# Performance work log

Hardware: AMD Instinct MI355X
Metric: run time of the kernel (lower is better)

Reference implementation:

```python
import jax, jax.numpy as jnp
import numpy as np

N = 50000      # nodes
E = 400000     # edges (before self-loops)
IN = 128       # in_channels
OUT = 64       # out_channels (per-head; concat=False averages heads)
HEADS = 8      # heads of first GAT layer; second layer has 1 head
NEG_SLOPE = 0.2


def _glorot(key, shape, fan_in, fan_out):
    s = jnp.sqrt(2.0 / (fan_in + fan_out)).astype(jnp.float32)
    return jax.random.normal(key, shape, jnp.float32) * s


def setup_inputs() -> dict:
    key = jax.random.key(0)
    ks = jax.random.split(key, 10)
    x = jax.random.normal(ks[0], (N, IN), jnp.float32)
    edge_index = jax.random.randint(ks[1], (2, E), 0, N)
    # layer 1: heads=HEADS, per-head dim OUT
    W1 = _glorot(ks[2], (IN, HEADS * OUT), IN, HEADS * OUT)
    att_src1 = _glorot(ks[3], (HEADS, OUT), OUT, 1)
    att_dst1 = _glorot(ks[4], (HEADS, OUT), OUT, 1)
    b1 = jnp.zeros((OUT,), jnp.float32)
    # layer 2: heads=1
    W2 = _glorot(ks[5], (OUT, 1 * OUT), OUT, OUT)
    att_src2 = _glorot(ks[6], (1, OUT), OUT, 1)
    att_dst2 = _glorot(ks[7], (1, OUT), OUT, 1)
    b2 = jnp.zeros((OUT,), jnp.float32)
    return dict(x=x, edge_index=edge_index, W1=W1, att_src1=att_src1,
                att_dst1=att_dst1, b1=b1, W2=W2, att_src2=att_src2,
                att_dst2=att_dst2, b2=b2)


def gat_conv(x, edge_index, W, att_src, att_dst, bias, heads, ch):
    """PyG GATConv with concat=False (mean over heads), add_self_loops=True."""
    n = x.shape[0]
    loop = jnp.arange(n, dtype=edge_index.dtype)
    src = jnp.concatenate([edge_index[0], loop])  # [E+N]
    dst = jnp.concatenate([edge_index[1], loop])
    h = (x @ W).reshape(n, heads, ch)                     # [N, H, C]
    a_s = jnp.sum(h * att_src, axis=-1)                   # [N, H]
    a_d = jnp.sum(h * att_dst, axis=-1)                   # [N, H]
    e = jax.nn.leaky_relu(a_s[src] + a_d[dst], NEG_SLOPE)  # [E+N, H]
    # numerically stable segment softmax over incoming edges of each dst node
    emax = jax.lax.stop_gradient(
        jax.ops.segment_max(e, dst, num_segments=n))       # [N, H]
    ee = jnp.exp(e - emax[dst])
    denom = jax.ops.segment_sum(ee, dst, num_segments=n)  # [N, H]
    alpha = ee / denom[dst]                                # [E+N, H]
    out = jax.ops.segment_sum(alpha[:, :, None] * h[src], dst,
                              num_segments=n)              # [N, H, C]
    return out.mean(axis=1) + bias                         # [N, C]


def reference(x, edge_index, W1, att_src1, att_dst1, b1,
              W2, att_src2, att_dst2, b2):
    h = gat_conv(x, edge_index, W1, att_src1, att_dst1, b1, HEADS, OUT)
    h = jax.nn.elu(h)
    return gat_conv(h, edge_index, W2, att_src2, att_dst2, b2, 1, OUT)
```

## Files before the change

### kernel.cpp

```cpp
#include <hip/hip_runtime.h>
#include <cstdint>
#include <cstddef>

#define NEG_SLOPE 0.2f

typedef short bf16x8 __attribute__((ext_vector_type(8)));
typedef float f32x4 __attribute__((ext_vector_type(4)));
typedef float f32x2 __attribute__((ext_vector_type(2)));

__device__ __forceinline__ unsigned short f2bf(float f) {
  unsigned u = __float_as_uint(f);
  u = u + 0x7FFFu + ((u >> 16) & 1u);
  return (unsigned short)(u >> 16);
}
__device__ __forceinline__ float bf2f(unsigned short b) {
  return __uint_as_float((unsigned)b << 16);
}
__device__ __forceinline__ f32x2 unpk(unsigned xv) {
  f32x2 r;
  r.x = __uint_as_float(xv << 16);
  r.y = __uint_as_float(xv & 0xFFFF0000u);
  return r;
}
__device__ __forceinline__ float rlf(float v, int l) {
  return __uint_as_float(
      (unsigned)__builtin_amdgcn_readlane((int)__float_as_uint(v), l));
}

__global__ __launch_bounds__(256) void prep_all(
    const int* __restrict__ ei, int* __restrict__ counts,
    int* __restrict__ posb,
    const float* __restrict__ x, unsigned short* __restrict__ xb,
    const float* __restrict__ W1, const float* __restrict__ att_s1,
    const float* __restrict__ att_d1, unsigned short* __restrict__ AsAdT,
    unsigned short* __restrict__ WbT,
    const float* __restrict__ W2, unsigned short* __restrict__ W2t,
    const float* __restrict__ att_s2, const float* __restrict__ att_d2,
    float* __restrict__ AsAd2,
    int E, int ET, int N, int B0, int B1) {
  int b = blockIdx.x, tid = threadIdx.x;
  if (b < B0) {
    int i = b * 256 + tid;
    if (i < ET) {
      int dst = (i < E) ? ei[E + i] : (i - E);
      int pos = atomicAdd(&counts[dst], 1);
      posb[i] = pos;
    }
    return;
  }
  b -= B0;
  if (b < B1) {
    int i = b * 256 + tid;
    if (i < N * 32) {
      float4 v = ((const float4*)x)[i];
      ushort4 o;
      o.x = f2bf(v.x); o.y = f2bf(v.y); o.z = f2bf(v.z); o.w = f2bf(v.w);
      ((ushort4*)xb)[i] = o;
    }
    return;
  }
  b -= B1;
  if (b < 8) {
    int i = b * 256 + tid;
    int o = i >> 7, k = i & 127, h = o & 7;
    const float* att = (o < 8) ? att_s1 : att_d1;
    float s = 0.f;
    for (int c = 0; c < 64; c++) s += W1[(size_t)k * 512 + h * 64 + c] * att[h * 64 + c];
    AsAdT[i] = f2bf(s);
    return;
  }
  b -= 8;
  if (b < 256) {
    int i = b * 256 + tid;
    int o = i >> 10, k = i & 1023, h = k >> 7, c = k & 127;
    WbT[i] = f2bf(W1[(size_t)c * 512 + h * 64 + o]);
    return;
  }
  b -= 256;
  if (b < 16) {
    int i = b * 256 + tid;
    if (i < 64 * 64) {
      int k = i >> 6, nn = i & 63;
      W2t[(size_t)nn * 64 + k] = f2bf(W2[i]);
    }
    return;
  }
  {
    int i = tid;
    if (i < 128) {
      int o = i >> 6, k = i & 63;
      const float* att = (o == 0) ? att_s2 : att_d2;
      float s = 0.f;
      for (int c = 0; c < 64; c++) s += W2[(size_t)k * 64 + c] * att[c];
      AsAd2[i] = s;
    }
  }
}

__global__ __launch_bounds__(1024) void scan_dots(
    const int* __restrict__ counts, int* __restrict__ offsets,
    const unsigned short* __restrict__ xb, const unsigned short* __restrict__ AsAdT,
    float* __restrict__ asd, int n) {
  if (blockIdx.x == 0) {
    __shared__ int sums[1024];
    int t = threadIdx.x;
    int chunk = (n + 1023) >> 10;
    int start = t * chunk;
    int end = min(start + chunk, n);
    int s = 0;
    for (int i = start; i < end; i++) s += counts[i];
    sums[t] = s;
    __syncthreads();
    for (int off = 1; off < 1024; off <<= 1) {
      int v = (t >= off) ? sums[t - off] : 0;
      __syncthreads();
      sums[t] += v;
      __syncthreads();
    }
    int run = sums[t] - s;
    for (int i = start; i < end; i++) { offsets[i] = run; run += counts[i]; }
    if (t == 1023) offsets[n] = sums[1023];
    return;
  }
  int tid = threadIdx.x;
  int wave = tid >> 6, lane = tid & 63;
  int q = lane >> 4, t = lane & 15;
  int row0 = (blockIdx.x - 1) * 256 + wave * 16;
  int arow = row0 + t; if (arow > n - 1) arow = n - 1;
  const bf16x8* aptr = (const bf16x8*)(xb + (size_t)arow * 128);
  const bf16x8* bptr = (const bf16x8*)(AsAdT + t * 128);
  f32x4 acc = (f32x4){0.f, 0.f, 0.f, 0.f};
  #pragma unroll
  for (int s = 0; s < 4; s++)
    acc = __builtin_amdgcn_mfma_f32_16x16x32_bf16(aptr[s * 4 + q], bptr[s * 4 + q],
                                                  acc, 0, 0, 0);
  #pragma unroll
  for (int r = 0; r < 4; r++) {
    int row = row0 + q * 4 + r;
    if (row < n) asd[row * 16 + t] = acc[r];
  }
}

__global__ __launch_bounds__(256) void fill_csr(
    const int* __restrict__ ei, const int* __restrict__ offsets,
    const int* __restrict__ posb, int* __restrict__ srcs, int E, int ET) {
  int i = blockIdx.x * 256 + threadIdx.x;
  if (i >= ET) return;
  int src, dst;
  if (i < E) { src = ei[i]; dst = ei[E + i]; } else { src = dst = i - E; }
  srcs[offsets[dst] + posb[i]] = src;
}

#define CONSUME8R(RV, W, ACC)                                         \
  _Pragma("unroll")                                                   \
  for (int k = 0; k < 8; k++) {                                       \
    f32x2 x2 = unpk(RV[k]);                                           \
    ACC[0] += x2 * rlf(W, k * 8 + 0);                                 \
    ACC[1] += x2 * rlf(W, k * 8 + 1);                                 \
    ACC[2] += x2 * rlf(W, k * 8 + 2);                                 \
    ACC[3] += x2 * rlf(W, k * 8 + 3);                                 \
    ACC[4] += x2 * rlf(W, k * 8 + 4);                                 \
    ACC[5] += x2 * rlf(W, k * 8 + 5);                                 \
    ACC[6] += x2 * rlf(W, k * 8 + 6);                                 \
    ACC[7] += x2 * rlf(W, k * 8 + 7);                                 \
  }

__global__ __launch_bounds__(1024, 8) void agg1_gemm(
    const int* __restrict__ offsets, const int* __restrict__ srcs,
    const float* __restrict__ asd, const unsigned short* __restrict__ xb,
    const unsigned short* __restrict__ WbT, const float* __restrict__ b1,
    const float* __restrict__ AsAd2, unsigned short* __restrict__ zb,
    float* __restrict__ as2, float* __restrict__ ad2, int N) {
  __shared__ unsigned short sh[16 * 1032];
  int tid = threadIdx.x;
  int wv = tid >> 6, lane = tid & 63;
  int nb = blockIdx.x;
  {
    int node = nb * 16 + wv;
    f32x2 acc[8];
    #pragma unroll
    for (int h = 0; h < 8; h++) acc[h] = (f32x2){0.f, 0.f};
    float wsl = 0.f;
    int beg = offsets[node], end = offsets[node + 1];
    int jl = end - 1;
    float adv = asd[(size_t)node * 16 + 8 + (lane & 7)];
    for (int cb = beg; cb < end; cb += 16) {
      int cnt = min(16, end - cb);
      int sAll = srcs[min(cb + (lane & 15), jl)];
      int swa = srcs[min(cb + (lane >> 3), jl)];
      float asva = asd[(size_t)swa * 16 + (lane & 7)];
      float asvb = 0.f;
      if (cnt > 8) {
        int swb = srcs[min(cb + 8 + (lane >> 3), jl)];
        asvb = asd[(size_t)swb * 16 + (lane & 7)];
      }
      unsigned rva[8], rvb[8];
      #pragma unroll
      for (int k = 0; k < 8; k++) {
        int se = __builtin_amdgcn_readlane(sAll, k);
        rva[k] = *(const unsigned*)&xb[(size_t)(unsigned)se * 128 + 2 * lane];
      }
      if (cnt > 8) {
        #pragma unroll
        for (int k = 0; k < 8; k++) {
          int se = __builtin_amdgcn_readlane(sAll, k + 8);
          rvb[k] = *(const unsigned*)&xb[(size_t)(unsigned)se * 128 + 2 * lane];
        }
      }
      float wa, wb = 0.f;
      {
        float v = asva + adv;
        v = (v > 0.f) ? v : NEG_SLOPE * v;
        wa = (cb + (lane >> 3) < end) ? __expf(v) : 0.f;
      }
      if (cnt > 8) {
        float v = asvb + adv;
        v = (v > 0.f) ? v : NEG_SLOPE * v;
        wb = (cb + 8 + (lane >> 3) < end) ? __expf(v) : 0.f;
      }
      wsl += wa + wb;
      CONSUME8R(rva, wa, acc);
      if (cnt > 8) { CONSUME8R(rvb, wb, acc); }
    }
    wsl += __shfl_xor(wsl, 8, 64);
    wsl += __shfl_xor(wsl, 16, 64);
    wsl += __shfl_xor(wsl, 32, 64);
    #pragma unroll
    for (int h = 0; h < 8; h++) {
      float tot = rlf(wsl, h);
      float iv = 0.125f / tot;
      unsigned o = (unsigned)f2bf(acc[h].x * iv) | ((unsigned)f2bf(acc[h].y * iv) << 16);
      *(unsigned*)&sh[wv * 1032 + h * 128 + 2 * lane] = o;
    }
  }
  __syncthreads();
  if (wv < 4) {
    int q = lane >> 4, t = lane & 15;
    f32x4 acc4 = (f32x4){0.f, 0.f, 0.f, 0.f};
    const unsigned short* bbase = WbT + (size_t)(wv * 16 + t) * 1024;
    #pragma unroll 8
    for (int s = 0; s < 32; s++) {
      bf16x8 af = *(const bf16x8*)&sh[t * 1032 + s * 32 + q * 8];
      bf16x8 bf = *(const bf16x8*)&bbase[s * 32 + q * 8];
      acc4 = __builtin_amdgcn_mfma_f32_16x16x32_bf16(af, bf, acc4, 0, 0, 0);
    }
    int col = wv * 16 + t;
    float bias = b1[col];
    float vs = AsAd2[col], vd = AsAd2[64 + col];
    #pragma unroll
    for (int r = 0; r < 4; r++) {
      int row = q * 4 + r;
      int node = nb * 16 + row;
      float v = acc4[r] + bias;
      v = (v > 0.f) ? v : (__expf(v) - 1.f);
      zb[(size_t)node * 64 + col] = f2bf(v);
      float s = v * vs, d = v * vd;
      #pragma unroll
      for (int off = 1; off < 16; off <<= 1) {
        s += __shfl_xor(s, off, 64);
        d += __shfl_xor(d, off, 64);
      }
      if (t == 0) {
        atomicAdd(&as2[node], s);
        atomicAdd(&ad2[node], d);
      }
    }
  }
}

__global__ __launch_bounds__(1024, 8) void agg2_gemm(
    const int* __restrict__ offsets, const int* __restrict__ srcs,
    const float* __restrict__ as2, const float* __restrict__ ad2,
    const unsigned short* __restrict__ zb, const unsigned short* __restrict__ W2t,
    const float* __restrict__ b2, float* __restrict__ out, int N) {
  __shared__ unsigned short sh[16 * 72];
  int tid = threadIdx.x;
  int wv = tid >> 6, lane = tid & 63;
  int nb = blockIdx.x;
  {
    int node = nb * 16 + wv;
    int half = lane >> 5;
    float adv = ad2[node];
    int beg = offsets[node], end = offsets[node + 1];
    int jl = end - 1;
    f32x2 acc = (f32x2){0.f, 0.f};
    float wsl = 0.f;
    for (int cb = beg; cb < end; cb += 16) {
      int cnt = min(16, end - cb);
      int sAll = srcs[min(cb + (lane & 15), jl)];
      float asv = as2[sAll];
      unsigned rv[8];
      #pragma unroll
      for (int k = 0; k < 4; k++) {
        int s0 = __builtin_amdgcn_readlane(sAll, 2 * k);
        int s1 = __builtin_amdgcn_readlane(sAll, 2 * k + 1);
        int se = half ? s1 : s0;
        rv[k] = *(const unsigned*)&zb[(size_t)(unsigned)se * 64 + 2 * (lane & 31)];
      }
      if (cnt > 8) {
        #pragma unroll
        for (int k = 4; k < 8; k++) {
          int s0 = __builtin_amdgcn_readlane(sAll, 2 * k);
          int s1 = __builtin_amdgcn_readlane(sAll, 2 * k + 1);
          int se = half ? s1 : s0;
          rv[k] = *(const unsigned*)&zb[(size_t)(unsigned)se * 64 + 2 * (lane & 31)];
        }
      }
      float v = asv + adv;
      v = (v > 0.f) ? v : NEG_SLOPE * v;
      float wl = (cb + (lane & 15) < end) ? __expf(v) : 0.f;
      if (lane < 16) wsl += wl;
      #pragma unroll
      for (int k = 0; k < 4; k++) {
        float w0 = rlf(wl, 2 * k);
        float w1 = rlf(wl, 2 * k + 1);
        float w = half ? w1 : w0;
        acc += unpk(rv[k]) * w;
      }
      if (cnt > 8) {
        #pragma unroll
        for (int k = 4; k < 8; k++) {
          float w0 = rlf(wl, 2 * k);
          float w1 = rlf(wl, 2 * k + 1);
          float w = half ? w1 : w0;
          acc += unpk(rv[k]) * w;
        }
      }
    }
    wsl += __shfl_xor(wsl, 1, 64);
    wsl += __shfl_xor(wsl, 2, 64);
    wsl += __shfl_xor(wsl, 4, 64);
    wsl += __shfl_xor(wsl, 8, 64);
    float tot = rlf(wsl, 0);
    acc.x += __shfl_xor(acc.x, 32, 64);
    acc.y += __shfl_xor(acc.y, 32, 64);
    if (lane < 32) {
      float inv = 1.f / tot;
      unsigned o = (unsigned)f2bf(acc.x * inv) | ((unsigned)f2bf(acc.y * inv) << 16);
      *(unsigned*)&sh[wv * 72 + 2 * lane] = o;
    }
  }
  __syncthreads();
  if (wv < 4) {
    int q = lane >> 4, t = lane & 15;
    f32x4 acc4 = (f32x4){0.f, 0.f, 0.f, 0.f};
    const unsigned short* bbase = W2t + (size_t)(wv * 16 + t) * 64;
    #pragma unroll
    for (int s = 0; s < 2; s++) {
      bf16x8 af = *(const bf16x8*)&sh[t * 72 + s * 32 + q * 8];
      bf16x8 bf = *(const bf16x8*)&bbase[s * 32 + q * 8];
      acc4 = __builtin_amdgcn_mfma_f32_16x16x32_bf16(af, bf, acc4, 0, 0, 0);
    }
    int col = wv * 16 + t;
    float bias = b2[col];
    #pragma unroll
    for (int r = 0; r < 4; r++) {
      int node = nb * 16 + q * 4 + r;
      if (node < N) out[(size_t)node * 64 + col] = acc4[r] + bias;
    }
  }
}

extern "C" void kernel_launch(void* const* d_in, const int* in_sizes, int n_in,
                              void* d_out, int out_size, void* d_ws, size_t ws_size,
                              hipStream_t stream) {
  const int IN = 128;
  const int N = in_sizes[0] / IN;
  const int E = in_sizes[1] / 2;
  const int ET = E + N;

  const float* x        = (const float*)d_in[0];
  const int*   ei       = (const int*)d_in[1];
  const float* W1       = (const float*)d_in[2];
  const float* att_src1 = (const float*)d_in[3];
  const float* att_dst1 = (const float*)d_in[4];
  const float* b1       = (const float*)d_in[5];
  const float* W2       = (const float*)d_in[6];
  const float* att_src2 = (const float*)d_in[7];
  const float* att_dst2 = (const float*)d_in[8];
  const float* b2       = (const float*)d_in[9];
  float* out = (float*)d_out;

  char* base = (char*)d_ws;
  size_t off = 0;
  auto alloc = [&](size_t bytes) -> char* {
    char* p = base + off;
    off = (off + bytes + 255) & ~(size_t)255;
    return p;
  };
  unsigned short* xb    = (unsigned short*)alloc((size_t)N * 128 * 2);
  unsigned short* AsAdT = (unsigned short*)alloc((size_t)16 * 128 * 2);
  unsigned short* WbT   = (unsigned short*)alloc((size_t)64 * 1024 * 2);
  unsigned short* W2t   = (unsigned short*)alloc((size_t)64 * 64 * 2);
  unsigned short* zb    = (unsigned short*)alloc((size_t)N * 64 * 2);
  float* AsAd2 = (float*)alloc((size_t)128 * 4);
  float* asd1  = (float*)alloc((size_t)N * 16 * 4);
  int* offsets = (int*)alloc((size_t)(N + 1) * 4);
  int* srcs    = (int*)alloc((size_t)ET * 4);
  int* posb    = (int*)alloc((size_t)ET * 4);
  char* zero_begin = base + off;
  int* counts  = (int*)alloc((size_t)N * 4);
  float* a_s2  = (float*)alloc((size_t)N * 4);
  float* a_d2  = (float*)alloc((size_t)N * 4);
  char* zero_end = base + off;

  hipMemsetAsync(zero_begin, 0, (size_t)(zero_end - zero_begin), stream);

  const int TB = 256;
  auto cdiv = [](int a, int b) { return (a + b - 1) / b; };

  int B0 = cdiv(ET, TB);
  int B1 = cdiv(N * 32, TB);
  prep_all<<<B0 + B1 + 8 + 256 + 16 + 1, TB, 0, stream>>>(
      ei, counts, posb, x, xb, W1, att_src1, att_dst1, AsAdT, WbT, W2, W2t,
      att_src2, att_dst2, AsAd2, E, ET, N, B0, B1);

  scan_dots<<<1 + cdiv(N, 256), 1024, 0, stream>>>(counts, offsets, xb, AsAdT,
                                                   asd1, N);

  fill_csr<<<cdiv(ET, TB), TB, 0, stream>>>(ei, offsets, posb, srcs, E, ET);

  agg1_gemm<<<cdiv(N, 16), 1024, 0, stream>>>(offsets, srcs, asd1, xb, WbT, b1,
                                              AsAd2, zb, a_s2, a_d2, N);

  agg2_gemm<<<cdiv(N, 16), 1024, 0, stream>>>(offsets, srcs, a_s2, a_d2, zb,
                                              W2t, b2, out, N);
}
```

Before: 305.1 us.

## Halve aggregation block size to 8 nodes and skip unused neighbor row loads

The two fused aggregate+GEMM kernels now use 512-thread blocks covering 8 destination nodes instead of 16. The MFMA tile still has 16 rows, so half the rows duplicate the shared-memory data and their results are masked off. Neighbor feature gathers are now done in groups of 4 and skipped when the chunk holds fewer edges, which avoids redundant clamped loads for low-degree nodes. The intent is to cut barrier wait on the slowest wave in a block and to save memory traffic, at the cost of wasting half of each MFMA tile and launching twice as many blocks.

```diff
diff --git a/kernel.cpp b/kernel.cpp
--- a/kernel.cpp
+++ b/kernel.cpp
@@ -165,18 +165,18 @@
     ACC[7] += x2 * rlf(W, k * 8 + 7);                                 \
   }
 
-__global__ __launch_bounds__(1024, 8) void agg1_gemm(
+__global__ __launch_bounds__(512, 8) void agg1_gemm(
     const int* __restrict__ offsets, const int* __restrict__ srcs,
     const float* __restrict__ asd, const unsigned short* __restrict__ xb,
     const unsigned short* __restrict__ WbT, const float* __restrict__ b1,
     const float* __restrict__ AsAd2, unsigned short* __restrict__ zb,
     float* __restrict__ as2, float* __restrict__ ad2, int N) {
-  __shared__ unsigned short sh[16 * 1032];
+  __shared__ unsigned short sh[8 * 1032];
   int tid = threadIdx.x;
   int wv = tid >> 6, lane = tid & 63;
   int nb = blockIdx.x;
   {
-    int node = nb * 16 + wv;
+    int node = nb * 8 + wv;
     f32x2 acc[8];
     #pragma unroll
     for (int h = 0; h < 8; h++) acc[h] = (f32x2){0.f, 0.f};
@@ -188,21 +188,36 @@
       int cnt = min(16, end - cb);
       int sAll = srcs[min(cb + (lane & 15), jl)];
       int swa = srcs[min(cb + (lane >> 3), jl)];
-      float asva = asd[(size_t)swa * 16 + (lane & 7)];
+      float asva = asd[(size_t)(unsigned)swa * 16 + (lane & 7)];
       float asvb = 0.f;
       if (cnt > 8) {
         int swb = srcs[min(cb + 8 + (lane >> 3), jl)];
-        asvb = asd[(size_t)swb * 16 + (lane & 7)];
-      }
-      unsigned rva[8], rvb[8];
+        asvb = asd[(size_t)(unsigned)swb * 16 + (lane & 7)];
+      }
+      unsigned rva[8] = {0, 0, 0, 0, 0, 0, 0, 0};
+      unsigned rvb[8] = {0, 0, 0, 0, 0, 0, 0, 0};
       #pragma unroll
-      for (int k = 0; k < 8; k++) {
+      for (int k = 0; k < 4; k++) {
         int se = __builtin_amdgcn_readlane(sAll, k);
         rva[k] = *(const unsigned*)&xb[(size_t)(unsigned)se * 128 + 2 * lane];
       }
+      if (cnt > 4) {
+        #pragma unroll
+        for (int k = 4; k < 8; k++) {
+          int se = __builtin_amdgcn_readlane(sAll, k);
+          rva[k] = *(const unsigned*)&xb[(size_t)(unsigned)se * 128 + 2 * lane];
+        }
+      }
       if (cnt > 8) {
         #pragma unroll
-        for (int k = 0; k < 8; k++) {
+        for (int k = 0; k < 4; k++) {
+          int se = __builtin_amdgcn_readlane(sAll, k + 8);
+          rvb[k] = *(const unsigned*)&xb[(size_t)(unsigned)se * 128 + 2 * lane];
+        }
+      }
+      if (cnt > 12) {
+        #pragma unroll
+        for (int k = 4; k < 8; k++) {
           int se = __builtin_amdgcn_readlane(sAll, k + 8);
           rvb[k] = *(const unsigned*)&xb[(size_t)(unsigned)se * 128 + 2 * lane];
         }
@@ -240,7 +255,7 @@
     const unsigned short* bbase = WbT + (size_t)(wv * 16 + t) * 1024;
     #pragma unroll 8
     for (int s = 0; s < 32; s++) {
-      bf16x8 af = *(const bf16x8*)&sh[t * 1032 + s * 32 + q * 8];
+      bf16x8 af = *(const bf16x8*)&sh[(t & 7) * 1032 + s * 32 + q * 8];
       bf16x8 bf = *(const bf16x8*)&bbase[s * 32 + q * 8];
       acc4 = __builtin_amdgcn_mfma_f32_16x16x32_bf16(af, bf, acc4, 0, 0, 0);
     }
@@ -250,35 +265,37 @@
     #pragma unroll
     for (int r = 0; r < 4; r++) {
       int row = q * 4 + r;
-      int node = nb * 16 + row;
       float v = acc4[r] + bias;
       v = (v > 0.f) ? v : (__expf(v) - 1.f);
-      zb[(size_t)node * 64 + col] = f2bf(v);
       float s = v * vs, d = v * vd;
       #pragma unroll
       for (int off = 1; off < 16; off <<= 1) {
         s += __shfl_xor(s, off, 64);
         d += __shfl_xor(d, off, 64);
       }
-      if (t == 0) {
-        atomicAdd(&as2[node], s);
-        atomicAdd(&ad2[node], d);
-      }
-    }
-  }
-}
-
-__global__ __launch_bounds__(1024, 8) void agg2_gemm(
+      if (row < 8) {
+        int node = nb * 8 + row;
+        zb[(size_t)node * 64 + col] = f2bf(v);
+        if (t == 0) {
+          atomicAdd(&as2[node], s);
+          atomicAdd(&ad2[node], d);
+        }
+      }
+    }
+  }
+}
+
+__global__ __launch_bounds__(512, 8) void agg2_gemm(
     const int* __restrict__ offsets, const int* __restrict__ srcs,
     const float* __restrict__ as2, const float* __restrict__ ad2,
     const unsigned short* __restrict__ zb, const unsigned short* __restrict__ W2t,
     const float* __restrict__ b2, float* __restrict__ out, int N) {
-  __shared__ unsigned short sh[16 * 72];
+  __shared__ unsigned short sh[8 * 72];
   int tid = threadIdx.x;
   int wv = tid >> 6, lane = tid & 63;
   int nb = blockIdx.x;
   {
-    int node = nb * 16 + wv;
+    int node = nb * 8 + wv;
     int half = lane >> 5;
     float adv = ad2[node];
     int beg = offsets[node], end = offsets[node + 1];
@@ -289,17 +306,35 @@
       int cnt = min(16, end - cb);
       int sAll = srcs[min(cb + (lane & 15), jl)];
       float asv = as2[sAll];
-      unsigned rv[8];
+      unsigned rv[8] = {0, 0, 0, 0, 0, 0, 0, 0};
       #pragma unroll
-      for (int k = 0; k < 4; k++) {
+      for (int k = 0; k < 2; k++) {
         int s0 = __builtin_amdgcn_readlane(sAll, 2 * k);
         int s1 = __builtin_amdgcn_readlane(sAll, 2 * k + 1);
         int se = half ? s1 : s0;
         rv[k] = *(const unsigned*)&zb[(size_t)(unsigned)se * 64 + 2 * (lane & 31)];
       }
+      if (cnt > 4) {
+        #pragma unroll
+        for (int k = 2; k < 4; k++) {
+          int s0 = __builtin_amdgcn_readlane(sAll, 2 * k);
+          int s1 = __builtin_amdgcn_readlane(sAll, 2 * k + 1);
+          int se = half ? s1 : s0;
+          rv[k] = *(const unsigned*)&zb[(size_t)(unsigned)se * 64 + 2 * (lane & 31)];
+        }
+      }
       if (cnt > 8) {
         #pragma unroll
-        for (int k = 4; k < 8; k++) {
+        for (int k = 4; k < 6; k++) {
+          int s0 = __builtin_amdgcn_readlane(sAll, 2 * k);
+          int s1 = __builtin_amdgcn_readlane(sAll, 2 * k + 1);
+          int se = half ? s1 : s0;
+          rv[k] = *(const unsigned*)&zb[(size_t)(unsigned)se * 64 + 2 * (lane & 31)];
+        }
+      }
+      if (cnt > 12) {
+        #pragma unroll
+        for (int k = 6; k < 8; k++) {
           int s0 = __builtin_amdgcn_readlane(sAll, 2 * k);
           int s1 = __builtin_amdgcn_readlane(sAll, 2 * k + 1);
           int se = half ? s1 : s0;
@@ -347,7 +382,7 @@
     const unsigned short* bbase = W2t + (size_t)(wv * 16 + t) * 64;
     #pragma unroll
     for (int s = 0; s < 2; s++) {
-      bf16x8 af = *(const bf16x8*)&sh[t * 72 + s * 32 + q * 8];
+      bf16x8 af = *(const bf16x8*)&sh[(t & 7) * 72 + s * 32 + q * 8];
       bf16x8 bf = *(const bf16x8*)&bbase[s * 32 + q * 8];
       acc4 = __builtin_amdgcn_mfma_f32_16x16x32_bf16(af, bf, acc4, 0, 0, 0);
     }
@@ -355,8 +390,11 @@
     float bias = b2[col];
     #pragma unroll
     for (int r = 0; r < 4; r++) {
-      int node = nb * 16 + q * 4 + r;
-      if (node < N) out[(size_t)node * 64 + col] = acc4[r] + bias;
+      int row = q * 4 + r;
+      if (row < 8) {
+        int node = nb * 8 + row;
+        if (node < N) out[(size_t)node * 64 + col] = acc4[r] + bias;
+      }
     }
   }
 }
@@ -420,9 +458,9 @@
 
   fill_csr<<<cdiv(ET, TB), TB, 0, stream>>>(ei, offsets, posb, srcs, E, ET);
 
-  agg1_gemm<<<cdiv(N, 16), 1024, 0, stream>>>(offsets, srcs, asd1, xb, WbT, b1,
-                                              AsAd2, zb, a_s2, a_d2, N);
-
-  agg2_gemm<<<cdiv(N, 16), 1024, 0, stream>>>(offsets, srcs, a_s2, a_d2, zb,
-                                              W2t, b2, out, N);
-}
+  agg1_gemm<<<cdiv(N, 8), 512, 0, stream>>>(offsets, srcs, asd1, xb, WbT, b1,
+                                            AsAd2, zb, a_s2, a_d2, N);
+
+  agg2_gemm<<<cdiv(N, 8), 512, 0, stream>>>(offsets, srcs, a_s2, a_d2, zb,
+                                            W2t, b2, out, N);
+}
```

Result: slower. 338.8 us (+11.1%).

## Process four node groups per block in agg1_gemm with double-buffered shared tiles

Applied to the files above, without the earlier changes.

agg1_gemm now handles 64 nodes per block in four 16-node groups. Each group's gather-aggregation result goes into one of two shared buffers, and a different set of four waves runs the MFMA projection for each group. This lets the GEMM of one group overlap with the aggregation of the next and spreads the MFMA work across waves instead of leaving 12 waves idle. The cost is a larger shared-memory footprint, which may reduce occupancy, plus a __syncthreads per group, added node clamping and bounds guards.

```diff
diff --git a/kernel.cpp b/kernel.cpp
--- a/kernel.cpp
+++ b/kernel.cpp
@@ -171,98 +171,105 @@
     const unsigned short* __restrict__ WbT, const float* __restrict__ b1,
     const float* __restrict__ AsAd2, unsigned short* __restrict__ zb,
     float* __restrict__ as2, float* __restrict__ ad2, int N) {
-  __shared__ unsigned short sh[16 * 1032];
+  __shared__ unsigned short sh[2][16 * 1032];
   int tid = threadIdx.x;
   int wv = tid >> 6, lane = tid & 63;
-  int nb = blockIdx.x;
-  {
-    int node = nb * 16 + wv;
-    f32x2 acc[8];
-    #pragma unroll
-    for (int h = 0; h < 8; h++) acc[h] = (f32x2){0.f, 0.f};
-    float wsl = 0.f;
-    int beg = offsets[node], end = offsets[node + 1];
-    int jl = end - 1;
-    float adv = asd[(size_t)node * 16 + 8 + (lane & 7)];
-    for (int cb = beg; cb < end; cb += 16) {
-      int cnt = min(16, end - cb);
-      int sAll = srcs[min(cb + (lane & 15), jl)];
-      int swa = srcs[min(cb + (lane >> 3), jl)];
-      float asva = asd[(size_t)swa * 16 + (lane & 7)];
-      float asvb = 0.f;
-      if (cnt > 8) {
-        int swb = srcs[min(cb + 8 + (lane >> 3), jl)];
-        asvb = asd[(size_t)swb * 16 + (lane & 7)];
-      }
-      unsigned rva[8], rvb[8];
+  int nbase = blockIdx.x * 64;
+  for (int g = 0; g < 4; ++g) {
+    unsigned short* zt = &sh[g & 1][0];
+    {
+      int node = min(nbase + g * 16 + wv, N - 1);
+      f32x2 acc[8];
       #pragma unroll
-      for (int k = 0; k < 8; k++) {
-        int se = __builtin_amdgcn_readlane(sAll, k);
-        rva[k] = *(const unsigned*)&xb[(size_t)(unsigned)se * 128 + 2 * lane];
-      }
-      if (cnt > 8) {
+      for (int h = 0; h < 8; h++) acc[h] = (f32x2){0.f, 0.f};
+      float wsl = 0.f;
+      int beg = offsets[node], end = offsets[node + 1];
+      int jl = end - 1;
+      float adv = asd[(size_t)node * 16 + 8 + (lane & 7)];
+      for (int cb = beg; cb < end; cb += 16) {
+        int cnt = min(16, end - cb);
+        int sAll = srcs[min(cb + (lane & 15), jl)];
+        int swa = srcs[min(cb + (lane >> 3), jl)];
+        float asva = asd[(size_t)(unsigned)swa * 16 + (lane & 7)];
+        float asvb = 0.f;
+        if (cnt > 8) {
+          int swb = srcs[min(cb + 8 + (lane >> 3), jl)];
+          asvb = asd[(size_t)(unsigned)swb * 16 + (lane & 7)];
+        }
+        unsigned rva[8], rvb[8];
         #pragma unroll
         for (int k = 0; k < 8; k++) {
-          int se = __builtin_amdgcn_readlane(sAll, k + 8);
-          rvb[k] = *(const unsigned*)&xb[(size_t)(unsigned)se * 128 + 2 * lane];
-        }
-      }
-      float wa, wb = 0.f;
-      {
-        float v = asva + adv;
-        v = (v > 0.f) ? v : NEG_SLOPE * v;
-        wa = (cb + (lane >> 3) < end) ? __expf(v) : 0.f;
-      }
-      if (cnt > 8) {
-        float v = asvb + adv;
-        v = (v > 0.f) ? v : NEG_SLOPE * v;
-        wb = (cb + 8 + (lane >> 3) < end) ? __expf(v) : 0.f;
-      }
-      wsl += wa + wb;
-      CONSUME8R(rva, wa, acc);
-      if (cnt > 8) { CONSUME8R(rvb, wb, acc); }
-    }
-    wsl += __shfl_xor(wsl, 8, 64);
-    wsl += __shfl_xor(wsl, 16, 64);
-    wsl += __shfl_xor(wsl, 32, 64);
-    #pragma unroll
-    for (int h = 0; h < 8; h++) {
-      float tot = rlf(wsl, h);
-      float iv = 0.125f / tot;
-      unsigned o = (unsigned)f2bf(acc[h].x * iv) | ((unsigned)f2bf(acc[h].y * iv) << 16);
-      *(unsigned*)&sh[wv * 1032 + h * 128 + 2 * lane] = o;
-    }
-  }
-  __syncthreads();
-  if (wv < 4) {
-    int q = lane >> 4, t = lane & 15;
-    f32x4 acc4 = (f32x4){0.f, 0.f, 0.f, 0.f};
-    const unsigned short* bbase = WbT + (size_t)(wv * 16 + t) * 1024;
-    #pragma unroll 8
-    for (int s = 0; s < 32; s++) {
-      bf16x8 af = *(const bf16x8*)&sh[t * 1032 + s * 32 + q * 8];
-      bf16x8 bf = *(const bf16x8*)&bbase[s * 32 + q * 8];
-      acc4 = __builtin_amdgcn_mfma_f32_16x16x32_bf16(af, bf, acc4, 0, 0, 0);
-    }
-    int col = wv * 16 + t;
-    float bias = b1[col];
-    float vs = AsAd2[col], vd = AsAd2[64 + col];
-    #pragma unroll
-    for (int r = 0; r < 4; r++) {
-      int row = q * 4 + r;
-      int node = nb * 16 + row;
-      float v = acc4[r] + bias;
-      v = (v > 0.f) ? v : (__expf(v) - 1.f);
-      zb[(size_t)node * 64 + col] = f2bf(v);
-      float s = v * vs, d = v * vd;
+          int se = __builtin_amdgcn_readlane(sAll, k);
+          rva[k] = *(const unsigned*)&xb[(size_t)(unsigned)se * 128 + 2 * lane];
+        }
+        if (cnt > 8) {
+          #pragma unroll
+          for (int k = 0; k < 8; k++) {
+            int se = __builtin_amdgcn_readlane(sAll, k + 8);
+            rvb[k] = *(const unsigned*)&xb[(size_t)(unsigned)se * 128 + 2 * lane];
+          }
+        }
+        float wa, wb = 0.f;
+        {
+          float v = asva + adv;
+          v = (v > 0.f) ? v : NEG_SLOPE * v;
+          wa = (cb + (lane >> 3) < end) ? __expf(v) : 0.f;
+        }
+        if (cnt > 8) {
+          float v = asvb + adv;
+          v = (v > 0.f) ? v : NEG_SLOPE * v;
+          wb = (cb + 8 + (lane >> 3) < end) ? __expf(v) : 0.f;
+        }
+        wsl += wa + wb;
+        CONSUME8R(rva, wa, acc);
+        if (cnt > 8) { CONSUME8R(rvb, wb, acc); }
+      }
+      wsl += __shfl_xor(wsl, 8, 64);
+      wsl += __shfl_xor(wsl, 16, 64);
+      wsl += __shfl_xor(wsl, 32, 64);
       #pragma unroll
-      for (int off = 1; off < 16; off <<= 1) {
-        s += __shfl_xor(s, off, 64);
-        d += __shfl_xor(d, off, 64);
-      }
-      if (t == 0) {
-        atomicAdd(&as2[node], s);
-        atomicAdd(&ad2[node], d);
+      for (int h = 0; h < 8; h++) {
+        float tot = rlf(wsl, h);
+        float iv = 0.125f / tot;
+        unsigned o = (unsigned)f2bf(acc[h].x * iv) |
+                     ((unsigned)f2bf(acc[h].y * iv) << 16);
+        *(unsigned*)&zt[wv * 1032 + h * 128 + 2 * lane] = o;
+      }
+    }
+    __syncthreads();
+    if ((wv >> 2) == g) {
+      int w4 = wv & 3;
+      int q = lane >> 4, t = lane & 15;
+      f32x4 acc4 = (f32x4){0.f, 0.f, 0.f, 0.f};
+      const unsigned short* bbase = WbT + (size_t)(w4 * 16 + t) * 1024;
+      #pragma unroll 8
+      for (int s = 0; s < 32; s++) {
+        bf16x8 af = *(const bf16x8*)&zt[t * 1032 + s * 32 + q * 8];
+        bf16x8 bf = *(const bf16x8*)&bbase[s * 32 + q * 8];
+        acc4 = __builtin_amdgcn_mfma_f32_16x16x32_bf16(af, bf, acc4, 0, 0, 0);
+      }
+      int col = w4 * 16 + t;
+      float bias = b1[col];
+      float vs = AsAd2[col], vd = AsAd2[64 + col];
+      #pragma unroll
+      for (int r = 0; r < 4; r++) {
+        int row = q * 4 + r;
+        int node = nbase + g * 16 + row;
+        float v = acc4[r] + bias;
+        v = (v > 0.f) ? v : (__expf(v) - 1.f);
+        float s = v * vs, d = v * vd;
+        #pragma unroll
+        for (int off = 1; off < 16; off <<= 1) {
+          s += __shfl_xor(s, off, 64);
+          d += __shfl_xor(d, off, 64);
+        }
+        if (node < N) {
+          zb[(size_t)node * 64 + col] = f2bf(v);
+          if (t == 0) {
+            atomicAdd(&as2[node], s);
+            atomicAdd(&ad2[node], d);
+          }
+        }
       }
     }
   }
@@ -420,7 +427,7 @@
 
   fill_csr<<<cdiv(ET, TB), TB, 0, stream>>>(ei, offsets, posb, srcs, E, ET);
 
-  agg1_gemm<<<cdiv(N, 16), 1024, 0, stream>>>(offsets, srcs, asd1, xb, WbT, b1,
+  agg1_gemm<<<cdiv(N, 64), 1024, 0, stream>>>(offsets, srcs, asd1, xb, WbT, b1,
                                               AsAd2, zb, a_s2, a_d2, N);
 
   agg2_gemm<<<cdiv(N, 16), 1024, 0, stream>>>(offsets, srcs, a_s2, a_d2, zb,
```

Result: slower. 345.0 us (+13.1%).
